# Kernel optimization log

Measured on AMD Instinct MI355X. Metric: run time of the kernel, lower is better.

## Reference

```python
import jax, jax.numpy as jnp
import numpy as np

N_NODES = 100000
N_EDGES = 800000
IN_DIM, HID_DIM, OUT_DIM = 128, 256, 128


def setup_inputs() -> dict:
    key = jax.random.key(0)
    k1, k2, k3, k4, k5 = jax.random.split(key, 5)
    x = jax.random.normal(k1, (N_NODES, IN_DIM), dtype=jnp.float32)
    edge_index = jax.random.randint(k2, (2, N_EDGES), 0, N_NODES, dtype=jnp.int64)
    edge_weight = jax.random.uniform(k3, (N_EDGES,), dtype=jnp.float32)
    W1 = jax.random.normal(k4, (IN_DIM, HID_DIM), dtype=jnp.float32) * 0.02
    b1 = jnp.zeros((HID_DIM,), dtype=jnp.float32)
    W2 = jax.random.normal(k5, (HID_DIM, OUT_DIM), dtype=jnp.float32) * 0.02
    b2 = jnp.zeros((OUT_DIM,), dtype=jnp.float32)
    return {"x": x, "edge_index": edge_index, "edge_weight": edge_weight,
            "W1": W1, "b1": b1, "W2": W2, "b2": b2}


def reference(x, edge_index, edge_weight, W1, b1, W2, b2):
    # GCNConv (normalize=True, add_self_loops=False), two layers with ReLU.
    # Dropout is identity at inference.
    row = edge_index[0]  # source nodes (E,)
    col = edge_index[1]  # target nodes (E,)
    n = x.shape[0]

    # Symmetric normalization: deg at target, norm = d^-1/2[row]*w*d^-1/2[col]
    deg = jax.ops.segment_sum(edge_weight, col, num_segments=n)  # (N,)
    dis = jnp.where(deg > 0, jax.lax.rsqrt(deg), 0.0)
    norm = dis[row] * edge_weight * dis[col]  # (E,)

    def gcn_conv(h, W, b):
        h = h @ W                                   # (N, F_out)
        msg = h[row] * norm[:, None]                # (E, F_out) gather+scale
        agg = jax.ops.segment_sum(msg, col, num_segments=n)  # scatter-add
        return agg + b

    h = jax.nn.relu(gcn_conv(x.astype(jnp.float32), W1, b1))
    return gcn_conv(h, W2, b2)
```

## Files before the change

kernel.cpp:

```cpp
#include <hip/hip_runtime.h>
#include <hip/hip_bf16.h>
#include <cstdint>
#include <cstddef>

#define N_NODES 100000
#define N_EDGES 800000
#define IN_DIM 128
#define HID_DIM 256
#define OUT_DIM 128

typedef __attribute__((ext_vector_type(8))) short bf16x8;
typedef __attribute__((ext_vector_type(4))) float f32x4;

__device__ __forceinline__ unsigned short f32_to_bf16(float f) {
    __hip_bfloat16 b = __float2bfloat16(f);
    return *reinterpret_cast<unsigned short*>(&b);
}
__device__ __forceinline__ float bf16_lo(uint32_t u) {
    uint32_t v = u << 16; return *reinterpret_cast<float*>(&v);
}
__device__ __forceinline__ float bf16_hi(uint32_t u) {
    uint32_t v = u & 0xffff0000u; return *reinterpret_cast<float*>(&v);
}

#define HIST_BLOCKS 3125
#define XB_BLOCKS 12500

__global__ void hist_prep_kernel(const int* __restrict__ ei,
                                 int* __restrict__ cnt,
                                 int* __restrict__ rank,
                                 const float* __restrict__ x,
                                 uint32_t* __restrict__ xb,
                                 const float* __restrict__ W1,
                                 unsigned short* __restrict__ W1F,
                                 const float* __restrict__ W2,
                                 unsigned short* __restrict__ W2F) {
    int b = blockIdx.x;
    if (b < HIST_BLOCKS) {
        int e = b * 256 + threadIdx.x;
        rank[e] = atomicAdd(&cnt[ei[N_EDGES + e]], 1);
        return;
    }
    b -= HIST_BLOCKS;
    if (b < XB_BLOCKS) {
        int i = b * 256 + threadIdx.x;
        float4 v = ((const float4*)x)[i];
        uint32_t lo = (uint32_t)f32_to_bf16(v.x) | ((uint32_t)f32_to_bf16(v.y) << 16);
        uint32_t hi = (uint32_t)f32_to_bf16(v.z) | ((uint32_t)f32_to_bf16(v.w) << 16);
        ((uint2*)xb)[i] = make_uint2(lo, hi);
    } else if (b < XB_BLOCKS + 128) {
        int idx = (b - XB_BLOCKS) * 256 + threadIdx.x;
        int j = idx & 7, lane = (idx >> 3) & 63;
        int nt = (idx >> 9) & 3, ks = (idx >> 11) & 3;
        int wc = (idx >> 13) & 1, nh = (idx >> 14) & 1;
        int fr = lane & 15, fq = lane >> 4;
        int row = nh * 128 + wc * 64 + nt * 16 + fr;
        int kk = ks * 32 + fq * 8 + j;
        W1F[idx] = f32_to_bf16(W1[kk * HID_DIM + row]);
    } else {
        int idx = (b - XB_BLOCKS - 128) * 256 + threadIdx.x;
        int j = idx & 7, lane = (idx >> 3) & 63;
        int nt = (idx >> 9) & 3, ks = (idx >> 11) & 3;
        int wc = (idx >> 13) & 1, nh = (idx >> 14) & 1;
        int fr = lane & 15, fq = lane >> 4;
        int n = wc * 64 + nt * 16 + fr;
        int kk = nh * 128 + ks * 32 + fq * 8 + j;
        W2F[idx] = f32_to_bf16(W2[kk * OUT_DIM + n]);
    }
}

__global__ void scan1_kernel(const int* __restrict__ in, int* __restrict__ out,
                             int* __restrict__ bsums, int n) {
    __shared__ int tmp[256];
    int t = threadIdx.x;
    int i = blockIdx.x * 256 + t;
    int v = (i < n) ? in[i] : 0;
    tmp[t] = v;
    __syncthreads();
    for (int off = 1; off < 256; off <<= 1) {
        int u = (t >= off) ? tmp[t - off] : 0;
        __syncthreads();
        tmp[t] += u;
        __syncthreads();
    }
    if (i < n) out[i] = tmp[t] - v;
    if (t == 255) bsums[blockIdx.x] = tmp[255];
}

__global__ void scan2_kernel(int* __restrict__ bsums, int nb) {
    __shared__ int tmp[512];
    int t = threadIdx.x;
    int v = (t < nb) ? bsums[t] : 0;
    tmp[t] = v;
    __syncthreads();
    for (int off = 1; off < 512; off <<= 1) {
        int u = (t >= off) ? tmp[t - off] : 0;
        __syncthreads();
        tmp[t] += u;
        __syncthreads();
    }
    if (t < nb) bsums[t] = tmp[t] - v;
}

__global__ void scan3_kernel(int* __restrict__ rowp, const int* __restrict__ bsums,
                             int n, int total) {
    int i = blockIdx.x * 256 + threadIdx.x;
    if (i == 0) rowp[n] = total;
    if (i >= n) return;
    rowp[i] += bsums[blockIdx.x];
}

__global__ void place_kernel(const int* __restrict__ ei,
                             const float* __restrict__ ew,
                             const int* __restrict__ rank,
                             const int* __restrict__ rowp,
                             int2* __restrict__ pairs) {
    int e = blockIdx.x * 256 + threadIdx.x;
    if (e >= N_EDGES) return;
    int c = ei[N_EDGES + e];
    int pos = rowp[c] + rank[e];
    pairs[pos] = make_int2(ei[e], __float_as_int(ew[e]));
}

__global__ void deg_dis_kernel(const int* __restrict__ rowp,
                               const int2* __restrict__ pairs,
                               float* __restrict__ dis) {
    int v = blockIdx.x * 256 + threadIdx.x;
    if (v >= N_NODES) return;
    int b = rowp[v], e = rowp[v + 1];
    float d = 0.f;
    for (int j = b; j < e; ++j) d += __int_as_float(pairs[j].y);
    dis[v] = d > 0.f ? rsqrtf(d) : 0.f;
}

__global__ void normalize_kernel(const int* __restrict__ rowp,
                                 int2* __restrict__ pairs,
                                 const float* __restrict__ dis) {
    int v = blockIdx.x * 256 + threadIdx.x;
    if (v >= N_NODES) return;
    float dv = dis[v];
    int b = rowp[v], e = rowp[v + 1];
    for (int j = b; j < e; ++j) {
        int2 p = pairs[j];
        p.y = __float_as_int(__int_as_float(p.y) * dis[p.x] * dv);
        pairs[j] = p;
    }
}

__device__ __forceinline__ void acc_edge(float w, uint4 u, float* a) {
    a[0] += w * bf16_lo(u.x); a[1] += w * bf16_hi(u.x);
    a[2] += w * bf16_lo(u.y); a[3] += w * bf16_hi(u.y);
    a[4] += w * bf16_lo(u.z); a[5] += w * bf16_hi(u.z);
    a[6] += w * bf16_lo(u.w); a[7] += w * bf16_hi(u.w);
}

template <bool OUT_BF16>
__global__ void aggregate_kernel(const uint4* __restrict__ feat,
                                 const int* __restrict__ rowp,
                                 const int2* __restrict__ pairs,
                                 void* __restrict__ out_v,
                                 const float* __restrict__ bias) {
    int gtid = blockIdx.x * blockDim.x + threadIdx.x;
    int node = gtid >> 4;
    int lane = threadIdx.x & 15;
    if (node >= N_NODES) return;
    int beg = rowp[node], end = rowp[node + 1];
    float a[8] = {};

    int j = beg;
    for (; j + 4 <= end; j += 4) {
        int2 p[4]; uint4 u[4];
        #pragma unroll
        for (int q = 0; q < 4; ++q) p[q] = pairs[j + q];
        #pragma unroll
        for (int q = 0; q < 4; ++q) u[q] = feat[(size_t)p[q].x * 16 + lane];
        #pragma unroll
        for (int q = 0; q < 4; ++q) acc_edge(__int_as_float(p[q].y), u[q], a);
    }
    if (j + 2 <= end) {
        int2 p0 = pairs[j], p1 = pairs[j + 1];
        uint4 u0 = feat[(size_t)p0.x * 16 + lane];
        uint4 u1 = feat[(size_t)p1.x * 16 + lane];
        acc_edge(__int_as_float(p0.y), u0, a);
        acc_edge(__int_as_float(p1.y), u1, a);
        j += 2;
    }
    if (j < end) {
        int2 p0 = pairs[j];
        uint4 u0 = feat[(size_t)p0.x * 16 + lane];
        acc_edge(__int_as_float(p0.y), u0, a);
    }
    if (bias) {
        float4 b0 = ((const float4*)bias)[lane * 2];
        float4 b1 = ((const float4*)bias)[lane * 2 + 1];
        a[0] += b0.x; a[1] += b0.y; a[2] += b0.z; a[3] += b0.w;
        a[4] += b1.x; a[5] += b1.y; a[6] += b1.z; a[7] += b1.w;
    }
    if (OUT_BF16) {
        uint4 o;
        o.x = (uint32_t)f32_to_bf16(a[0]) | ((uint32_t)f32_to_bf16(a[1]) << 16);
        o.y = (uint32_t)f32_to_bf16(a[2]) | ((uint32_t)f32_to_bf16(a[3]) << 16);
        o.z = (uint32_t)f32_to_bf16(a[4]) | ((uint32_t)f32_to_bf16(a[5]) << 16);
        o.w = (uint32_t)f32_to_bf16(a[6]) | ((uint32_t)f32_to_bf16(a[7]) << 16);
        ((uint4*)out_v)[(size_t)node * 16 + lane] = o;
    } else {
        ((float4*)out_v)[(size_t)node * 32 + lane * 2] =
            make_float4(a[0], a[1], a[2], a[3]);
        ((float4*)out_v)[(size_t)node * 32 + lane * 2 + 1] =
            make_float4(a[4], a[5], a[6], a[7]);
    }
}

__global__ __launch_bounds__(256, 2) void gemm_fused_kernel(
    const unsigned short* __restrict__ A,
    const unsigned short* __restrict__ W1F,
    const float* __restrict__ b1,
    const unsigned short* __restrict__ W2F,
    unsigned short* __restrict__ T,
    int M) {
    __shared__ unsigned short As[128 * 128];
    __shared__ unsigned short Hs[128 * 136];
    int tid = threadIdx.x;
    int wave = tid >> 6, lane = tid & 63;
    int m0 = blockIdx.x * 128;
    int wr = (wave & 1) * 64;
    int wcid = wave >> 1;
    int wc = wcid * 64;
    int fr = lane & 15, fq = lane >> 4;

    #pragma unroll
    for (int i = 0; i < 8; ++i) {
        int cbase = (i * 4 + wave) * 64;
        int c = cbase + lane;
        int m = c >> 4, cl = c & 15;
        int qg = ((cl & 7) ^ (m & 7)) | (cl & 8);
        int gm = m0 + m; if (gm >= M) gm = M - 1;
        const unsigned short* ga = A + (size_t)gm * 128 + qg * 8;
        __builtin_amdgcn_global_load_lds(
            (const __attribute__((address_space(1))) void*)ga,
            (__attribute__((address_space(3))) void*)(As + (size_t)cbase * 8),
            16, 0, 0);
    }
    __syncthreads();

    bf16x8 af[4][4];
    #pragma unroll
    for (int ks = 0; ks < 4; ++ks) {
        int q = ks * 4 + fq;
        int cl = ((q & 7) ^ (fr & 7)) | (q & 8);
        #pragma unroll
        for (int mt = 0; mt < 4; ++mt)
            af[ks][mt] = *(const bf16x8*)(As + (wr + mt * 16 + fr) * 128 + cl * 8);
    }

    const bf16x8* w1p = (const bf16x8*)W1F;
    const bf16x8* w2p = (const bf16x8*)W2F;

    f32x4 acc_t[4][4] = {};
    #pragma unroll
    for (int nh = 0; nh < 2; ++nh) {
        int wbase = (nh * 2 + wcid) * 16 * 64;
        f32x4 acc_h[4][4] = {};
        #pragma unroll
        for (int ks = 0; ks < 4; ++ks) {
            bf16x8 wf[4];
            #pragma unroll
            for (int nt = 0; nt < 4; ++nt)
                wf[nt] = w1p[wbase + (ks * 4 + nt) * 64 + lane];
            #pragma unroll
            for (int mt = 0; mt < 4; ++mt)
                #pragma unroll
                for (int nt = 0; nt < 4; ++nt)
                    acc_h[mt][nt] = __builtin_amdgcn_mfma_f32_16x16x32_bf16(
                        af[ks][mt], wf[nt], acc_h[mt][nt], 0, 0, 0);
        }
        float bv[4];
        #pragma unroll
        for (int nt = 0; nt < 4; ++nt) bv[nt] = b1[nh * 128 + wc + nt * 16 + fr];
        __syncthreads();
        #pragma unroll
        for (int mt = 0; mt < 4; ++mt)
            #pragma unroll
            for (int r = 0; r < 4; ++r) {
                int row = wr + mt * 16 + fq * 4 + r;
                #pragma unroll
                for (int nt = 0; nt < 4; ++nt) {
                    float v = fmaxf(acc_h[mt][nt][r] + bv[nt], 0.f);
                    Hs[row * 136 + wc + nt * 16 + fr] = f32_to_bf16(v);
                }
            }
        __syncthreads();
        #pragma unroll
        for (int ks = 0; ks < 4; ++ks) {
            bf16x8 wf[4], hf[4];
            #pragma unroll
            for (int nt = 0; nt < 4; ++nt)
                wf[nt] = w2p[wbase + (ks * 4 + nt) * 64 + lane];
            #pragma unroll
            for (int mt = 0; mt < 4; ++mt)
                hf[mt] = *(const bf16x8*)(Hs + (wr + mt * 16 + fr) * 136 + ks * 32 + fq * 8);
            #pragma unroll
            for (int mt = 0; mt < 4; ++mt)
                #pragma unroll
                for (int nt = 0; nt < 4; ++nt)
                    acc_t[mt][nt] = __builtin_amdgcn_mfma_f32_16x16x32_bf16(
                        hf[mt], wf[nt], acc_t[mt][nt], 0, 0, 0);
        }
    }

    #pragma unroll
    for (int mt = 0; mt < 4; ++mt)
        #pragma unroll
        for (int r = 0; r < 4; ++r) {
            int row = m0 + wr + mt * 16 + fq * 4 + r;
            if (row >= M) continue;
            #pragma unroll
            for (int nt = 0; nt < 4; ++nt)
                T[(size_t)row * 128 + wc + nt * 16 + fr] = f32_to_bf16(acc_t[mt][nt][r]);
        }
}

extern "C" void kernel_launch(void* const* d_in, const int* in_sizes, int n_in,
                              void* d_out, int out_size, void* d_ws, size_t ws_size,
                              hipStream_t stream) {
    const float* x  = (const float*)d_in[0];
    const int*   ei = (const int*)d_in[1];
    const float* ew = (const float*)d_in[2];
    const float* W1 = (const float*)d_in[3];
    const float* b1 = (const float*)d_in[4];
    const float* W2 = (const float*)d_in[5];
    const float* b2 = (const float*)d_in[6];
    float* out = (float*)d_out;

    char* ws = (char*)d_ws;
    size_t off = 0;
    auto alloc = [&](size_t bytes) -> void* {
        void* p = ws + off;
        off = (off + bytes + 255) & ~(size_t)255;
        return p;
    };
    int*   cnt   = (int*)  alloc((size_t)N_NODES * 4);
    float* dis   = (float*)alloc((size_t)N_NODES * 4);
    int*   rowp  = (int*)  alloc((size_t)(N_NODES + 1) * 4);
    int*   bsums = (int*)  alloc(512 * 4);
    int*   rank  = (int*)  alloc((size_t)N_EDGES * 4);
    int2*  pairs = (int2*) alloc((size_t)N_EDGES * 8);
    uint32_t* xb = (uint32_t*)alloc((size_t)N_NODES * IN_DIM * 2);
    unsigned short* W1F = (unsigned short*)alloc((size_t)IN_DIM * HID_DIM * 2);
    unsigned short* W2F = (unsigned short*)alloc((size_t)HID_DIM * OUT_DIM * 2);
    unsigned short* A1  = (unsigned short*)alloc((size_t)N_NODES * IN_DIM * 2);
    unsigned short* t   = (unsigned short*)alloc((size_t)N_NODES * OUT_DIM * 2);

    hipMemsetAsync(cnt, 0, (size_t)N_NODES * 4, stream);

    int nn_blocks = (N_NODES + 255) / 256;
    int ne_blocks = (N_EDGES + 255) / 256;

    hist_prep_kernel<<<HIST_BLOCKS + XB_BLOCKS + 256, 256, 0, stream>>>(
        ei, cnt, rank, x, xb, W1, W1F, W2, W2F);

    scan1_kernel<<<nn_blocks, 256, 0, stream>>>(cnt, rowp, bsums, N_NODES);
    scan2_kernel<<<1, 512, 0, stream>>>(bsums, nn_blocks);
    scan3_kernel<<<nn_blocks, 256, 0, stream>>>(rowp, bsums, N_NODES, N_EDGES);
    place_kernel<<<ne_blocks, 256, 0, stream>>>(ei, ew, rank, rowp, pairs);
    deg_dis_kernel<<<nn_blocks, 256, 0, stream>>>(rowp, pairs, dis);
    normalize_kernel<<<nn_blocks, 256, 0, stream>>>(rowp, pairs, dis);

    int agg_blocks = (N_NODES * 16) / 256;

    aggregate_kernel<true><<<agg_blocks, 256, 0, stream>>>(
        (const uint4*)xb, rowp, pairs, A1, nullptr);

    gemm_fused_kernel<<<(N_NODES + 127) / 128, 256, 0, stream>>>(
        A1, W1F, b1, W2F, t, N_NODES);

    aggregate_kernel<false><<<agg_blocks, 256, 0, stream>>>(
        (const uint4*)t, rowp, pairs, out, b2);
}
```

Baseline: 281.8 us.

## Fuse degree computation into histogram atomics and merge scan and normalize kernels

The histogram pass now packs the edge count and a fixed-point weight sum into one 64-bit atomic per edge, so degrees come out of the same pass. The first scan kernel computes the inverse square root degree, the second and third scan kernels merge into one that reduces the block sums directly, and edge placement applies the normalization inline. This removes the separate degree and normalize passes and two launches. The aggregate loop is also unrolled to eight edges. The cost is fixed-point rounding of the degree and wider 64-bit atomics.

```diff
diff --git a/kernel.cpp b/kernel.cpp
--- a/kernel.cpp
+++ b/kernel.cpp
@@ -9,6 +9,9 @@
 #define HID_DIM 256
 #define OUT_DIM 128
 
+#define DEG_SCALE 2097152.0f
+#define DEG_INV   (1.0f / 2097152.0f)
+
 typedef __attribute__((ext_vector_type(8))) short bf16x8;
 typedef __attribute__((ext_vector_type(4))) float f32x4;
 
@@ -27,7 +30,8 @@
 #define XB_BLOCKS 12500
 
 __global__ void hist_prep_kernel(const int* __restrict__ ei,
-                                 int* __restrict__ cnt,
+                                 const float* __restrict__ ew,
+                                 unsigned long long* __restrict__ cnt64,
                                  int* __restrict__ rank,
                                  const float* __restrict__ x,
                                  uint32_t* __restrict__ xb,
@@ -38,7 +42,11 @@
     int b = blockIdx.x;
     if (b < HIST_BLOCKS) {
         int e = b * 256 + threadIdx.x;
-        rank[e] = atomicAdd(&cnt[ei[N_EDGES + e]], 1);
+        int c = ei[N_EDGES + e];
+        uint32_t wfix = (uint32_t)(ew[e] * DEG_SCALE + 0.5f);
+        unsigned long long add = (1ULL << 32) | (unsigned long long)wfix;
+        unsigned long long old = atomicAdd(&cnt64[c], add);
+        rank[e] = (int)(old >> 32);
         return;
     }
     b -= HIST_BLOCKS;
@@ -69,12 +77,14 @@
     }
 }
 
-__global__ void scan1_kernel(const int* __restrict__ in, int* __restrict__ out,
-                             int* __restrict__ bsums, int n) {
+__global__ void scan1_kernel(const unsigned long long* __restrict__ cnt64,
+                             int* __restrict__ out, int* __restrict__ bsums,
+                             float* __restrict__ dis, int n) {
     __shared__ int tmp[256];
     int t = threadIdx.x;
     int i = blockIdx.x * 256 + t;
-    int v = (i < n) ? in[i] : 0;
+    unsigned long long cv = (i < n) ? cnt64[i] : 0ULL;
+    int v = (int)(cv >> 32);
     tmp[t] = v;
     __syncthreads();
     for (int off = 1; off < 256; off <<= 1) {
@@ -83,68 +93,45 @@
         tmp[t] += u;
         __syncthreads();
     }
-    if (i < n) out[i] = tmp[t] - v;
+    if (i < n) {
+        out[i] = tmp[t] - v;
+        uint32_t wf = (uint32_t)cv;
+        dis[i] = wf ? rsqrtf((float)wf * DEG_INV) : 0.f;
+    }
     if (t == 255) bsums[blockIdx.x] = tmp[255];
 }
 
-__global__ void scan2_kernel(int* __restrict__ bsums, int nb) {
-    __shared__ int tmp[512];
-    int t = threadIdx.x;
-    int v = (t < nb) ? bsums[t] : 0;
-    tmp[t] = v;
+__global__ void scan23_kernel(int* __restrict__ rowp, const int* __restrict__ bsums,
+                              int n, int total) {
+    __shared__ int red[256];
+    int b = blockIdx.x, t = threadIdx.x;
+    int s = 0;
+    for (int i = t; i < b; i += 256) s += bsums[i];
+    red[t] = s;
     __syncthreads();
-    for (int off = 1; off < 512; off <<= 1) {
-        int u = (t >= off) ? tmp[t - off] : 0;
-        __syncthreads();
-        tmp[t] += u;
-        __syncthreads();
-    }
-    if (t < nb) bsums[t] = tmp[t] - v;
-}
-
-__global__ void scan3_kernel(int* __restrict__ rowp, const int* __restrict__ bsums,
-                             int n, int total) {
-    int i = blockIdx.x * 256 + threadIdx.x;
+    for (int off = 128; off > 0; off >>= 1) {
+        if (t < off) red[t] += red[t + off];
+        __syncthreads();
+    }
+    int pre = red[0];
+    int i = b * 256 + t;
     if (i == 0) rowp[n] = total;
-    if (i >= n) return;
-    rowp[i] += bsums[blockIdx.x];
+    if (i < n) rowp[i] += pre;
 }
 
 __global__ void place_kernel(const int* __restrict__ ei,
                              const float* __restrict__ ew,
                              const int* __restrict__ rank,
                              const int* __restrict__ rowp,
+                             const float* __restrict__ dis,
                              int2* __restrict__ pairs) {
     int e = blockIdx.x * 256 + threadIdx.x;
     if (e >= N_EDGES) return;
+    int s = ei[e];
     int c = ei[N_EDGES + e];
     int pos = rowp[c] + rank[e];
-    pairs[pos] = make_int2(ei[e], __float_as_int(ew[e]));
-}
-
-__global__ void deg_dis_kernel(const int* __restrict__ rowp,
-                               const int2* __restrict__ pairs,
-                               float* __restrict__ dis) {
-    int v = blockIdx.x * 256 + threadIdx.x;
-    if (v >= N_NODES) return;
-    int b = rowp[v], e = rowp[v + 1];
-    float d = 0.f;
-    for (int j = b; j < e; ++j) d += __int_as_float(pairs[j].y);
-    dis[v] = d > 0.f ? rsqrtf(d) : 0.f;
-}
-
-__global__ void normalize_kernel(const int* __restrict__ rowp,
-                                 int2* __restrict__ pairs,
-                                 const float* __restrict__ dis) {
-    int v = blockIdx.x * 256 + threadIdx.x;
-    if (v >= N_NODES) return;
-    float dv = dis[v];
-    int b = rowp[v], e = rowp[v + 1];
-    for (int j = b; j < e; ++j) {
-        int2 p = pairs[j];
-        p.y = __float_as_int(__int_as_float(p.y) * dis[p.x] * dv);
-        pairs[j] = p;
-    }
+    float wn = ew[e] * dis[s] * dis[c];
+    pairs[pos] = make_int2(s, __float_as_int(wn));
 }
 
 __device__ __forceinline__ void acc_edge(float w, uint4 u, float* a) {
@@ -168,7 +155,16 @@
     float a[8] = {};
 
     int j = beg;
-    for (; j + 4 <= end; j += 4) {
+    for (; j + 8 <= end; j += 8) {
+        int2 p[8]; uint4 u[8];
+        #pragma unroll
+        for (int q = 0; q < 8; ++q) p[q] = pairs[j + q];
+        #pragma unroll
+        for (int q = 0; q < 8; ++q) u[q] = feat[(size_t)p[q].x * 16 + lane];
+        #pragma unroll
+        for (int q = 0; q < 8; ++q) acc_edge(__int_as_float(p[q].y), u[q], a);
+    }
+    if (j + 4 <= end) {
         int2 p[4]; uint4 u[4];
         #pragma unroll
         for (int q = 0; q < 4; ++q) p[q] = pairs[j + q];
@@ -176,6 +172,7 @@
         for (int q = 0; q < 4; ++q) u[q] = feat[(size_t)p[q].x * 16 + lane];
         #pragma unroll
         for (int q = 0; q < 4; ++q) acc_edge(__int_as_float(p[q].y), u[q], a);
+        j += 4;
     }
     if (j + 2 <= end) {
         int2 p0 = pairs[j], p1 = pairs[j + 1];
@@ -339,7 +336,7 @@
         off = (off + bytes + 255) & ~(size_t)255;
         return p;
     };
-    int*   cnt   = (int*)  alloc((size_t)N_NODES * 4);
+    unsigned long long* cnt64 = (unsigned long long*)alloc((size_t)N_NODES * 8);
     float* dis   = (float*)alloc((size_t)N_NODES * 4);
     int*   rowp  = (int*)  alloc((size_t)(N_NODES + 1) * 4);
     int*   bsums = (int*)  alloc(512 * 4);
@@ -351,20 +348,17 @@
     unsigned short* A1  = (unsigned short*)alloc((size_t)N_NODES * IN_DIM * 2);
     unsigned short* t   = (unsigned short*)alloc((size_t)N_NODES * OUT_DIM * 2);
 
-    hipMemsetAsync(cnt, 0, (size_t)N_NODES * 4, stream);
+    hipMemsetAsync(cnt64, 0, (size_t)N_NODES * 8, stream);
 
     int nn_blocks = (N_NODES + 255) / 256;
     int ne_blocks = (N_EDGES + 255) / 256;
 
     hist_prep_kernel<<<HIST_BLOCKS + XB_BLOCKS + 256, 256, 0, stream>>>(
-        ei, cnt, rank, x, xb, W1, W1F, W2, W2F);
-
-    scan1_kernel<<<nn_blocks, 256, 0, stream>>>(cnt, rowp, bsums, N_NODES);
-    scan2_kernel<<<1, 512, 0, stream>>>(bsums, nn_blocks);
-    scan3_kernel<<<nn_blocks, 256, 0, stream>>>(rowp, bsums, N_NODES, N_EDGES);
-    place_kernel<<<ne_blocks, 256, 0, stream>>>(ei, ew, rank, rowp, pairs);
-    deg_dis_kernel<<<nn_blocks, 256, 0, stream>>>(rowp, pairs, dis);
-    normalize_kernel<<<nn_blocks, 256, 0, stream>>>(rowp, pairs, dis);
+        ei, ew, cnt64, rank, x, xb, W1, W1F, W2, W2F);
+
+    scan1_kernel<<<nn_blocks, 256, 0, stream>>>(cnt64, rowp, bsums, dis, N_NODES);
+    scan23_kernel<<<nn_blocks, 256, 0, stream>>>(rowp, bsums, N_NODES, N_EDGES);
+    place_kernel<<<ne_blocks, 256, 0, stream>>>(ei, ew, rank, rowp, dis, pairs);
 
     int agg_blocks = (N_NODES * 16) / 256;
 
```

New measurement: 277.2 us. Within noise of the previous version (-1.7%).
